# Performance work log

Measured on AMD Instinct MI355X. Metric: run time of the kernel, lower is better.

The kernel has to match this reference:

```python
import jax, jax.numpy as jnp
import numpy as np

DIM = 256
N_CHANNELS = 8
NEIGHBORS = 16


def setup_inputs() -> dict:
    key = jax.random.key(0)
    kx, kw = jax.random.split(key)
    B, N, D = 4, 1024, DIM
    x = jax.random.normal(kx, (B, N, D), dtype=jnp.float32)
    # nn.Linear(dim, dim*2*n_channels, bias=False); store as [in, out] so y = x @ W
    W_qk = jax.random.normal(kw, (D, 2 * N_CHANNELS * D), dtype=jnp.float32) * (D ** -0.5)
    return {"x": x, "W_qk": W_qk}


def _norm_edge(edge):
    # edge: [B, C, N, N]
    norm_row = edge / (edge.sum(axis=-1, keepdims=True) + 1e-6)
    norm_col = norm_row / (norm_row.sum(axis=-2, keepdims=True) + 1e-6)
    # norm_row @ norm_col^T
    return jnp.einsum('bcnk,bcmk->bcnm', norm_row, norm_col)


def reference(x, W_qk):
    B, N, D = x.shape
    C = N_CHANNELS
    scale = D ** -0.5
    qk = (x @ W_qk).reshape(B, N, 2, C, D)
    q = jnp.transpose(qk[:, :, 0], (0, 2, 1, 3))  # [B, C, N, D]
    k = jnp.transpose(qk[:, :, 1], (0, 2, 1, 3))  # [B, C, N, D]
    attn = jax.nn.softmax(jnp.einsum('bcnd,bcmd->bcnm', q, k) * scale, axis=-1)

    # clip(): top-k neighbor mask from channel-summed (detached) attention
    sum_edge = jax.lax.stop_gradient(attn).sum(axis=1)  # [B, N, N]
    kk = min(NEIGHBORS, N)
    _, top_idx = jax.lax.top_k(sum_edge, kk)  # [B, N, kk]
    b_idx = jnp.arange(B)[:, None, None]
    r_idx = jnp.arange(N)[None, :, None]
    mask = jnp.zeros((B, N, N), dtype=attn.dtype).at[b_idx, r_idx, top_idx].set(1.0)
    mask = jnp.maximum(mask, jnp.eye(N, dtype=attn.dtype))  # identity diag
    edge = mask[:, None] * attn  # [B, C, N, N]
    return _norm_edge(edge)
```

## Files before the change

kernel.cpp:

```cpp
#include <hip/hip_runtime.h>
#include <hip/hip_bf16.h>
#include <math.h>

#define BB 4
#define NN 1024
#define DD 256
#define CC 8
#define KNBR 16
#define MAXSEL 17
#define ZCAP (NN * MAXSEL)

typedef _Float16 f16x8_t __attribute__((ext_vector_type(8)));
typedef _Float16 f16x4_t __attribute__((ext_vector_type(4)));
typedef float    f32x4_t __attribute__((ext_vector_type(4)));

__device__ __forceinline__ void gl2lds16(const _Float16* g, _Float16* ldsbase) {
    __builtin_amdgcn_global_load_lds(
        (const __attribute__((address_space(1))) unsigned int*)g,
        (__attribute__((address_space(3))) unsigned int*)ldsbase, 16, 0, 0);
}

__device__ __forceinline__ void split2(float v, _Float16& h, _Float16& l) {
    h = (_Float16)v;
    l = (_Float16)(v - (float)h);
}

__global__ __launch_bounds__(256) void split_all(const float* __restrict__ x,
                                                 const float* __restrict__ W,
                                                 _Float16* __restrict__ xh,
                                                 _Float16* __restrict__ xl,
                                                 _Float16* __restrict__ Wth,
                                                 _Float16* __restrict__ Wtl,
                                                 int* __restrict__ countb) {
    const int tid = threadIdx.x;
    if (blockIdx.x < 1024) {
        int i = (blockIdx.x * 256 + tid) * 4;
        float4 v = *(const float4*)(x + i);
        f16x4_t hv, lv;
        _Float16 h, l;
        split2(v.x, h, l); hv[0] = h; lv[0] = l;
        split2(v.y, h, l); hv[1] = h; lv[1] = l;
        split2(v.z, h, l); hv[2] = h; lv[2] = l;
        split2(v.w, h, l); hv[3] = h; lv[3] = l;
        *(f16x4_t*)(xh + i) = hv;
        *(f16x4_t*)(xl + i) = lv;
    } else {
        const int b2 = blockIdx.x - 1024;
        if (b2 == 0) {
            int4 zz = make_int4(0, 0, 0, 0);
#pragma unroll
            for (int g = 0; g < 4; g++) ((int4*)countb)[tid + 256 * g] = zz;
        }
        __shared__ float t[64][65];
        const int n0 = (b2 & 63) * 64;
        const int k0 = (b2 >> 6) * 64;
#pragma unroll
        for (int i = 0; i < 16; i++) {
            int k = i * 4 + (tid >> 6);
            int n = tid & 63;
            t[k][n] = W[(size_t)(k0 + k) * 4096 + n0 + n];
        }
        __syncthreads();
#pragma unroll
        for (int i = 0; i < 16; i++) {
            int n = i * 4 + (tid >> 6);
            int k = tid & 63;
            _Float16 h, l;
            split2(t[k][n] * 16.f, h, l);
            size_t o = (size_t)(n0 + n) * 256 + k0 + k;
            Wth[o] = h; Wtl[o] = l;
        }
    }
}

#define STG(dst, src, rowbase, kk)                                             \
    do {                                                                       \
        gl2lds16((src) + (size_t)((rowbase) + r_st) * 256 + (kk) + c8,         \
                 &(dst)[(w * 64) * 8]);                                        \
        gl2lds16((src) + (size_t)((rowbase) + 64 + r_st) * 256 + (kk) + c8,    \
                 &(dst)[(256 + w * 64) * 8]);                                  \
    } while (0)

#define MFMA3(accv, AH, AL, BH, BL)                                            \
    do {                                                                       \
        accv = __builtin_amdgcn_mfma_f32_16x16x32_f16(AL, BH, accv, 0, 0, 0);  \
        accv = __builtin_amdgcn_mfma_f32_16x16x32_f16(AH, BL, accv, 0, 0, 0);  \
        accv = __builtin_amdgcn_mfma_f32_16x16x32_f16(AH, BH, accv, 0, 0, 0);  \
    } while (0)

#define COMPUTE(AH, AL, BH, BL)                                                \
    do {                                                                       \
        f16x8_t ah[4], al[4];                                                  \
        _Pragma("unroll")                                                      \
        for (int mi = 0; mi < 4; mi++) {                                       \
            int r = (wr * 64 + mi * 16 + lm) * 32 + qx8;                       \
            ah[mi] = *(const f16x8_t*)&(AH)[r];                                \
            al[mi] = *(const f16x8_t*)&(AL)[r];                                \
        }                                                                      \
        _Pragma("unroll")                                                      \
        for (int ni = 0; ni < 4; ni++) {                                       \
            int rb = (wc * 64 + ni * 16 + lm) * 32 + qx8;                      \
            f16x8_t bh = *(const f16x8_t*)&(BH)[rb];                           \
            f16x8_t bl = *(const f16x8_t*)&(BL)[rb];                           \
            _Pragma("unroll")                                                  \
            for (int mi = 0; mi < 4; mi++)                                     \
                MFMA3(acc[mi][ni], ah[mi], al[mi], bh, bl);                    \
        }                                                                      \
    } while (0)

__global__ __launch_bounds__(256) void gemm_xw_mfma(
        const _Float16* __restrict__ xh, const _Float16* __restrict__ xl,
        const _Float16* __restrict__ wth, const _Float16* __restrict__ wtl,
        _Float16* __restrict__ qh, _Float16* __restrict__ ql,
        _Float16* __restrict__ kh, _Float16* __restrict__ kl) {
    __shared__ __align__(16) char smem[65536];
    _Float16* Ah0 = (_Float16*)smem;
    _Float16* Al0 = (_Float16*)(smem + 8192);
    _Float16* Bh0 = (_Float16*)(smem + 16384);
    _Float16* Bl0 = (_Float16*)(smem + 24576);
    _Float16* Ah1 = (_Float16*)(smem + 32768);
    _Float16* Al1 = (_Float16*)(smem + 40960);
    _Float16* Bh1 = (_Float16*)(smem + 49152);
    _Float16* Bl1 = (_Float16*)(smem + 57344);
    const int tid = threadIdx.x, lane = tid & 63, w = tid >> 6;
    const int wr = w >> 1, wc = w & 1;
    const int lm = lane & 15, quad = lane >> 4;
    const int row0 = blockIdx.y * 128, col0 = blockIdx.x * 128;
    const int r_st = tid >> 2;
    const int c8 = (((tid & 3) ^ ((tid >> 3) & 3)) * 8);
    const int qx8 = ((quad ^ ((lm >> 1) & 3)) * 8);

    f32x4_t acc[4][4];
#pragma unroll
    for (int i = 0; i < 4; i++)
#pragma unroll
        for (int j = 0; j < 4; j++) acc[i][j] = (f32x4_t)(0.f);

    STG(Ah0, xh, row0, 0); STG(Al0, xl, row0, 0);
    STG(Bh0, wth, col0, 0); STG(Bl0, wtl, col0, 0);
    __syncthreads();
#pragma unroll
    for (int t = 0; t < 8; t += 2) {
        {
            int kn = (t + 1) * 32;
            if (t + 1 < 8) {
                STG(Ah1, xh, row0, kn); STG(Al1, xl, row0, kn);
                STG(Bh1, wth, col0, kn); STG(Bl1, wtl, col0, kn);
            }
            COMPUTE(Ah0, Al0, Bh0, Bl0);
            __syncthreads();
        }
        {
            int kn = (t + 2) * 32;
            if (t + 2 < 8) {
                STG(Ah0, xh, row0, kn); STG(Al0, xl, row0, kn);
                STG(Bh0, wth, col0, kn); STG(Bl0, wtl, col0, kn);
            }
            COMPUTE(Ah1, Al1, Bh1, Bl1);
            __syncthreads();
        }
    }

    float* tr = (float*)smem;
    const int s = col0 >> 11, c = (col0 >> 8) & 7, dbase = col0 & 255;
    _Float16* dh = s ? kh : qh;
    _Float16* dl = s ? kl : ql;
    const int rl = tid >> 2;
    const int cb = (tid & 3) * 8;
#pragma unroll
    for (int p = 0; p < 2; p++) {
        if (p) __syncthreads();
        if (wr == p) {
#pragma unroll
            for (int mi = 0; mi < 4; mi++) {
                int rloc = mi * 16 + quad * 4;
#pragma unroll
                for (int ni = 0; ni < 4; ni++) {
                    int cl = wc * 64 + ni * 16 + lm;
#pragma unroll
                    for (int r = 0; r < 4; r++)
                        tr[(rloc + r) * 132 + cl] = acc[mi][ni][r];
                }
            }
        }
        __syncthreads();
        int rr = row0 + p * 64 + rl;
        int bb = rr >> 10, n = rr & 1023;
        size_t base = (((size_t)(bb * CC + c)) * NN + n) * DD + dbase;
#pragma unroll
        for (int g = 0; g < 4; g++) {
            int ccol = g * 32 + cb;
            f16x8_t hv, lv;
#pragma unroll
            for (int e = 0; e < 8; e++) {
                float vv = tr[rl * 132 + ccol + e];
                _Float16 h, l;
                split2(vv, h, l);
                hv[e] = h; lv[e] = l;
            }
            *(f16x8_t*)(dh + base + ccol) = hv;
            *(f16x8_t*)(dl + base + ccol) = lv;
        }
    }
}

__global__ __launch_bounds__(256) void gemm_qkt_mfma(
        const _Float16* __restrict__ qh, const _Float16* __restrict__ ql,
        const _Float16* __restrict__ kh, const _Float16* __restrict__ kl,
        float* __restrict__ attn) {
    __shared__ __align__(16) char smem[65536];
    _Float16* Ah0 = (_Float16*)smem;
    _Float16* Al0 = (_Float16*)(smem + 8192);
    _Float16* Bh0 = (_Float16*)(smem + 16384);
    _Float16* Bl0 = (_Float16*)(smem + 24576);
    _Float16* Ah1 = (_Float16*)(smem + 32768);
    _Float16* Al1 = (_Float16*)(smem + 40960);
    _Float16* Bh1 = (_Float16*)(smem + 49152);
    _Float16* Bl1 = (_Float16*)(smem + 57344);
    const int tid = threadIdx.x, lane = tid & 63, w = tid >> 6;
    const int wr = w >> 1, wc = w & 1;
    const int lm = lane & 15, quad = lane >> 4;
    const int id = blockIdx.x;
    const int rb8 = id & 7, qq = id >> 3;
    const int j = qq & 63, zhi = qq >> 6;
    const int z = zhi * 8 + rb8;
    const int row0 = (j >> 3) * 128, col0 = (j & 7) * 128;
    const size_t zo = (size_t)z * NN * DD;
    float* Cm = attn + (size_t)z * NN * NN;
    const int r_st = tid >> 2;
    const int c8 = (((tid & 3) ^ ((tid >> 3) & 3)) * 8);
    const int qx8 = ((quad ^ ((lm >> 1) & 3)) * 8);
    const float scale = 0.0625f / 256.0f;

    f32x4_t acc[4][4];
#pragma unroll
    for (int i = 0; i < 4; i++)
#pragma unroll
        for (int j2 = 0; j2 < 4; j2++) acc[i][j2] = (f32x4_t)(0.f);

    const _Float16* qhz = qh + zo;
    const _Float16* qlz = ql + zo;
    const _Float16* khz = kh + zo;
    const _Float16* klz = kl + zo;

    STG(Ah0, qhz, row0, 0); STG(Al0, qlz, row0, 0);
    STG(Bh0, khz, col0, 0); STG(Bl0, klz, col0, 0);
    __syncthreads();
#pragma unroll
    for (int t = 0; t < 8; t += 2) {
        {
            int kn = (t + 1) * 32;
            if (t + 1 < 8) {
                STG(Ah1, qhz, row0, kn); STG(Al1, qlz, row0, kn);
                STG(Bh1, khz, col0, kn); STG(Bl1, klz, col0, kn);
            }
            COMPUTE(Ah0, Al0, Bh0, Bl0);
            __syncthreads();
        }
        {
            int kn = (t + 2) * 32;
            if (t + 2 < 8) {
                STG(Ah0, qhz, row0, kn); STG(Al0, qlz, row0, kn);
                STG(Bh0, khz, col0, kn); STG(Bl0, klz, col0, kn);
            }
            COMPUTE(Ah1, Al1, Bh1, Bl1);
            __syncthreads();
        }
    }

#pragma unroll
    for (int mi = 0; mi < 4; mi++)
#pragma unroll
        for (int ni = 0; ni < 4; ni++) {
            int row = row0 + wr * 64 + mi * 16 + quad * 4;
            int col = col0 + wc * 64 + ni * 16 + lm;
#pragma unroll
            for (int r = 0; r < 4; r++)
                Cm[(size_t)(row + r) * NN + col] = acc[mi][ni][r] * scale;
        }
}

__global__ __launch_bounds__(256) void softmax_topk(const float* __restrict__ attn,
                                                    float2* __restrict__ ml,
                                                    int* __restrict__ idx,
                                                    int* __restrict__ cnt,
                                                    int* __restrict__ countb,
                                                    float* __restrict__ colsum) {
    __shared__ float psum[4][1280];
    __shared__ int fsel[MAXSEL];
    __shared__ int fcnt;
    const int bn = blockIdx.x, b = bn >> 10, n = bn & 1023;
    const int tid = threadIdx.x, lane = tid & 63, w = tid >> 6;

    if (tid < CC) colsum[(size_t)(b * CC + tid) * NN + n] = 0.f;

    const int colb = lane * 16;
    const int pb   = lane * 20;
    float4 u[2][4];
#pragma unroll
    for (int p = 0; p < 2; p++) {
        const int c = w * 2 + p;
        const float* rowp = attn + (((size_t)(b * CC + c) * NN + n) * NN) + colb;
#pragma unroll
        for (int g = 0; g < 4; g++) u[p][g] = *(const float4*)(rowp + g * 4);
    }

    float acc[16];
#pragma unroll
    for (int e = 0; e < 16; e++) acc[e] = 0.f;

#pragma unroll
    for (int p = 0; p < 2; p++) {
        const int c = w * 2 + p;
        const float* f = (const float*)&u[p][0];
        float mx = f[0];
#pragma unroll
        for (int e = 1; e < 16; e++) mx = fmaxf(mx, f[e]);
#pragma unroll
        for (int off = 1; off < 64; off <<= 1) mx = fmaxf(mx, __shfl_xor(mx, off));
        float sm = 0.f;
        float pe[16];
#pragma unroll
        for (int e = 0; e < 16; e++) { pe[e] = expf(f[e] - mx); sm += pe[e]; }
#pragma unroll
        for (int off = 1; off < 64; off <<= 1) sm += __shfl_xor(sm, off);
        if (lane == 0) ml[(size_t)(b * CC + c) * NN + n] = make_float2(mx, sm);
        float inv = 1.0f / sm;
#pragma unroll
        for (int e = 0; e < 16; e++) acc[e] += pe[e] * inv;
    }
#pragma unroll
    for (int g = 0; g < 4; g++)
        *(float4*)&psum[w][pb + g * 4] =
            make_float4(acc[g * 4], acc[g * 4 + 1], acc[g * 4 + 2], acc[g * 4 + 3]);
    __syncthreads();

    const int p4 = tid * 4 + (tid >> 2) * 4;
    float4 a0 = *(const float4*)&psum[0][p4];
    float4 a1 = *(const float4*)&psum[1][p4];
    float4 a2 = *(const float4*)&psum[2][p4];
    float4 a3 = *(const float4*)&psum[3][p4];
    float4 vs;
    vs.x = a0.x + a1.x + a2.x + a3.x;
    vs.y = a0.y + a1.y + a2.y + a3.y;
    vs.z = a0.z + a1.z + a2.z + a3.z;
    vs.w = a0.w + a1.w + a2.w + a3.w;
    *(float4*)&psum[0][p4] = vs;
    __syncthreads();

    if (w == 0) {
        unsigned vb[16];
#pragma unroll
        for (int g = 0; g < 4; g++) {
            float4 t4 = *(const float4*)&psum[0][pb + g * 4];
            vb[g * 4 + 0] = __float_as_uint(t4.x);
            vb[g * 4 + 1] = __float_as_uint(t4.y);
            vb[g * 4 + 2] = __float_as_uint(t4.z);
            vb[g * 4 + 3] = __float_as_uint(t4.w);
        }
        unsigned lo = 0u, hi = 0x7F800000u;
        while (lo < hi) {
            unsigned mid = lo + ((hi - lo) >> 1);
            int c = 0;
#pragma unroll
            for (int e = 0; e < 16; e++)
                c += (int)__popcll(__ballot(vb[e] > mid));
            if (c <= 15) hi = mid; else lo = mid + 1;
        }
        const unsigned V = hi;
        int cgt = 0, ceq = 0;
#pragma unroll
        for (int e = 0; e < 16; e++) {
            cgt += (vb[e] > V) ? 1 : 0;
            ceq += (vb[e] == V) ? 1 : 0;
        }
        int pk = cgt | (ceq << 16);
        int incl = pk;
#pragma unroll
        for (int o = 1; o < 64; o <<= 1) {
            int v2 = __shfl_up(incl, o);
            if (lane >= o) incl += v2;
        }
        int tot = __shfl(incl, 63);
        int c1 = tot & 0xffff;
        int need = KNBR - c1;
        int excl = incl - pk;
        int pg = excl & 0xffff;
        int pe2 = excl >> 16;
        int lg = 0, le = 0;
#pragma unroll
        for (int e = 0; e < 16; e++) {
            if (vb[e] > V) {
                fsel[pg + lg] = colb + e; lg++;
            } else if (vb[e] == V) {
                if (pe2 + le < need) fsel[c1 + pe2 + le] = colb + e;
                le++;
            }
        }
        if (lane == 0) {
            bool has = false;
#pragma unroll
            for (int t2 = 0; t2 < KNBR; t2++)
                if (fsel[t2] == n) has = true;
            int c = KNBR;
            if (!has) { fsel[KNBR] = n; c = KNBR + 1; }
            fcnt = c;
            cnt[bn] = c;
        }
    }
    __syncthreads();
    if (tid < fcnt) {
        idx[bn * MAXSEL + tid] = fsel[tid];
        atomicAdd(&countb[b * NN + fsel[tid]], 1);
    }
}

__global__ __launch_bounds__(256) void scan_offb(const int* __restrict__ countb,
                                                 int* __restrict__ offb,
                                                 int* __restrict__ curs,
                                                 const int* __restrict__ cnt,
                                                 const int* __restrict__ idx,
                                                 int* __restrict__ eidx,
                                                 int* __restrict__ pmap) {
    __shared__ int wtot[4];
    const int b = blockIdx.x, tid = threadIdx.x, lane = tid & 63, w = tid >> 6;
    int c0 = countb[b * NN + tid * 4 + 0];
    int c1 = countb[b * NN + tid * 4 + 1];
    int c2 = countb[b * NN + tid * 4 + 2];
    int c3 = countb[b * NN + tid * 4 + 3];
    int tsum = c0 + c1 + c2 + c3;
    int incl = tsum;
#pragma unroll
    for (int off = 1; off < 64; off <<= 1) {
        int v = __shfl_up(incl, off);
        if (lane >= off) incl += v;
    }
    if (lane == 63) wtot[w] = incl;
    __syncthreads();
    int woff = 0;
    for (int i = 0; i < w; i++) woff += wtot[i];
    int base = woff + incl - tsum;
    int o0 = base, o1 = base + c0, o2 = base + c0 + c1, o3 = base + c0 + c1 + c2;
    offb[b * NN + tid * 4 + 0] = o0;
    offb[b * NN + tid * 4 + 1] = o1;
    offb[b * NN + tid * 4 + 2] = o2;
    offb[b * NN + tid * 4 + 3] = o3;
    curs[b * NN + tid * 4 + 0] = o0;
    curs[b * NN + tid * 4 + 1] = o1;
    curs[b * NN + tid * 4 + 2] = o2;
    curs[b * NN + tid * 4 + 3] = o3;
    __syncthreads();

    for (int r = 0; r < 4; r++) {
        int n = tid + r * 256;
        int bn = b * NN + n;
        int c_ = cnt[bn];
        int start = n & 15;
        for (int jj = 0; jj < MAXSEL; jj++) {
            if (jj < c_) {
                int j = jj + start;
                if (j >= c_) j -= c_;
                int k = idx[bn * MAXSEL + j];
                int p = atomicAdd(&curs[b * NN + k], 1);
                eidx[b * ZCAP + p] = n;
                pmap[bn * MAXSEL + j] = p;
            }
        }
    }
}

__global__ __launch_bounds__(256) void rownorm_fill(const float* __restrict__ attn,
                                                    const float2* __restrict__ ml,
                                                    const int* __restrict__ idx,
                                                    const int* __restrict__ cnt,
                                                    const int* __restrict__ pmap,
                                                    float* __restrict__ nr,
                                                    float* __restrict__ colsum,
                                                    float* __restrict__ eval8) {
    const int t = blockIdx.x * 256 + threadIdx.x;
    const int z = t >> 10, n = t & 1023;
    const int b = z >> 3, c = z & 7;
    const int bn = b * NN + n;
    const int c_ = cnt[bn];
    const float* arow = attn + (size_t)t * NN;
    const float2 MM = ml[t];
    const float invl = 1.0f / MM.y;
    float a[MAXSEL];
    int kk[MAXSEL];
    float s = 0.f;
#pragma unroll
    for (int j = 0; j < MAXSEL; j++) {
        if (j < c_) {
            kk[j] = idx[bn * MAXSEL + j];
            float p = expf(arow[kk[j]] - MM.x) * invl;
            a[j] = p; s += p;
        }
    }
    const float inv = 1.f / (s + 1e-6f);
#pragma unroll
    for (int j = 0; j < MAXSEL; j++) {
        if (j < c_) {
            float v = a[j] * inv;
            nr[(size_t)t * MAXSEL + j] = v;
            atomicAdd(&colsum[(size_t)z * NN + kk[j]], v);
            int p = pmap[bn * MAXSEL + j];
            eval8[((size_t)b * ZCAP + p) * 8 + c] = v;
        }
    }
}

__global__ __launch_bounds__(512) void out_sparse(const float* __restrict__ nr,
                                                  const int* __restrict__ idx,
                                                  const int* __restrict__ cnt,
                                                  const int* __restrict__ offb,
                                                  const int* __restrict__ countb,
                                                  const float* __restrict__ colsum,
                                                  const int* __restrict__ eidx,
                                                  const float* __restrict__ eval8,
                                                  float* __restrict__ out) {
    __shared__ float acc[CC][NN];
    __shared__ float scm[CC][MAXSEL];
    __shared__ int goffs[MAXSEL];
    __shared__ int glens[MAXSEL];
    const int bn = blockIdx.x;
    const int b = bn >> 10, n = bn & 1023;
    const int tid = threadIdx.x, lane = tid & 63, w = tid >> 6;
    const int c_ = cnt[bn];

    f32x4_t zz = (f32x4_t)(0.f);
#pragma unroll
    for (int q = 0; q < 4; q++) ((f32x4_t*)acc)[tid + q * 512] = zz;

    if (tid < 256) {
        int c = tid >> 5, j = tid & 31;
        if (j < MAXSEL) {
            float sc = 0.f;
            if (j < c_) {
                int z = b * CC + c;
                int k = idx[bn * MAXSEL + j];
                float wgt = nr[((size_t)z * NN + n) * MAXSEL + j];
                sc = wgt / (colsum[(size_t)z * NN + k] + 1e-6f);
            }
            scm[c][j] = sc;
        }
    } else if (tid < 256 + MAXSEL) {
        int j = tid - 256;
        int off = 0, len = 0;
        if (j < c_) {
            int k = idx[bn * MAXSEL + j];
            off = offb[b * NN + k];
            len = countb[b * NN + k];
        }
        goffs[j] = off; glens[j] = len;
    }
    __syncthreads();

    for (int j = w; j < c_; j += 8) {
        const int off = goffs[j], len = glens[j];
        const float s0 = scm[0][j], s1 = scm[1][j], s2 = scm[2][j], s3 = scm[3][j];
        const float s4 = scm[4][j], s5 = scm[5][j], s6 = scm[6][j], s7 = scm[7][j];
        for (int l = lane; l < len; l += 64) {
            int m = eidx[b * ZCAP + off + l];
            const float* vp = eval8 + ((size_t)b * ZCAP + off + l) * 8;
            f32x4_t va = *(const f32x4_t*)vp;
            f32x4_t vb2 = *(const f32x4_t*)(vp + 4);
            atomicAdd(&acc[0][m], s0 * va[0]);
            atomicAdd(&acc[1][m], s1 * va[1]);
            atomicAdd(&acc[2][m], s2 * va[2]);
            atomicAdd(&acc[3][m], s3 * va[3]);
            atomicAdd(&acc[4][m], s4 * vb2[0]);
            atomicAdd(&acc[5][m], s5 * vb2[1]);
            atomicAdd(&acc[6][m], s6 * vb2[2]);
            atomicAdd(&acc[7][m], s7 * vb2[3]);
        }
    }
    __syncthreads();

#pragma unroll
    for (int q = 0; q < 4; q++) {
        int i4 = tid + q * 512;
        int c = i4 >> 8, m4 = i4 & 255;
        *(f32x4_t*)(out + ((size_t)(b * CC + c) * NN + n) * NN + m4 * 4) =
            ((f32x4_t*)acc)[i4];
    }
}

extern "C" void kernel_launch(void* const* d_in, const int* in_sizes, int n_in,
                              void* d_out, int out_size, void* d_ws, size_t ws_size,
                              hipStream_t stream) {
    const float* x = (const float*)d_in[0];
    const float* W = (const float*)d_in[1];
    float* out = (float*)d_out;
    char* ws = (char*)d_ws;

    float* attn = (float*)d_out;

    _Float16* qh  = (_Float16*)(ws);
    _Float16* ql  = (_Float16*)(ws + 16777216ull);
    _Float16* kh  = (_Float16*)(ws + 33554432ull);
    _Float16* kl  = (_Float16*)(ws + 50331648ull);
    _Float16* xh  = (_Float16*)(ws + 67108864ull);
    _Float16* xl  = (_Float16*)(ws + 69206016ull);
    _Float16* wth = (_Float16*)(ws + 71303168ull);
    _Float16* wtl = (_Float16*)(ws + 73400320ull);
    int*    idx  = (int*)   (ws + 75497472ull);
    int*    cnt  = (int*)   (ws + 75776000ull);
    float*  nr   = (float*) (ws + 75792384ull);
    float*  colsum = (float*)(ws + 78020608ull);
    float2* ml   = (float2*)(ws + 78151680ull);
    int*    countb = (int*) (ws + 78413824ull);
    int*    offb = (int*)   (ws + 78430208ull);
    int*    curs = (int*)   (ws + 78446592ull);
    int*    eidx = (int*)   (ws + 78577664ull);
    float*  eval8 = (float*)(ws + 78856192ull);
    int*    pmap = (int*)   (ws + 81084416ull);

    split_all<<<1280, 256, 0, stream>>>(x, W, xh, xl, wth, wtl, countb);
    gemm_xw_mfma<<<dim3(32, 32), 256, 0, stream>>>(xh, xl, wth, wtl,
                                                   qh, ql, kh, kl);
    gemm_qkt_mfma<<<2048, 256, 0, stream>>>(qh, ql, kh, kl, attn);
    softmax_topk<<<4096, 256, 0, stream>>>(attn, ml, idx, cnt, countb, colsum);
    scan_offb<<<4, 256, 0, stream>>>(countb, offb, curs, cnt, idx, eidx, pmap);
    rownorm_fill<<<128, 256, 0, stream>>>(attn, ml, idx, cnt, pmap, nr, colsum,
                                          eval8);
    out_sparse<<<4096, 512, 0, stream>>>(nr, idx, cnt, offb, countb, colsum,
                                         eidx, eval8, out);
}
```

Baseline: 415.2 us.

## Split scatter fill into wider kernel and shrink edge arrays to 16-bit

```diff
diff --git a/kernel.cpp b/kernel.cpp
--- a/kernel.cpp
+++ b/kernel.cpp
@@ -417,11 +417,7 @@
 
 __global__ __launch_bounds__(256) void scan_offb(const int* __restrict__ countb,
                                                  int* __restrict__ offb,
-                                                 int* __restrict__ curs,
-                                                 const int* __restrict__ cnt,
-                                                 const int* __restrict__ idx,
-                                                 int* __restrict__ eidx,
-                                                 int* __restrict__ pmap) {
+                                                 int* __restrict__ curs) {
     __shared__ int wtot[4];
     const int b = blockIdx.x, tid = threadIdx.x, lane = tid & 63, w = tid >> 6;
     int c0 = countb[b * NN + tid * 4 + 0];
@@ -449,22 +445,26 @@
     curs[b * NN + tid * 4 + 1] = o1;
     curs[b * NN + tid * 4 + 2] = o2;
     curs[b * NN + tid * 4 + 3] = o3;
-    __syncthreads();
-
-    for (int r = 0; r < 4; r++) {
-        int n = tid + r * 256;
-        int bn = b * NN + n;
-        int c_ = cnt[bn];
-        int start = n & 15;
-        for (int jj = 0; jj < MAXSEL; jj++) {
-            if (jj < c_) {
-                int j = jj + start;
-                if (j >= c_) j -= c_;
-                int k = idx[bn * MAXSEL + j];
-                int p = atomicAdd(&curs[b * NN + k], 1);
-                eidx[b * ZCAP + p] = n;
-                pmap[bn * MAXSEL + j] = p;
-            }
+}
+
+__global__ __launch_bounds__(64) void fill_struct(const int* __restrict__ cnt,
+                                                  const int* __restrict__ idx,
+                                                  int* __restrict__ curs,
+                                                  unsigned short* __restrict__ eidx16,
+                                                  int* __restrict__ pmap) {
+    const int b = blockIdx.x >> 4;
+    const int n = ((blockIdx.x & 15) << 6) + threadIdx.x;
+    const int bn = b * NN + n;
+    const int c_ = cnt[bn];
+    const int start = n & 15;
+    for (int jj = 0; jj < MAXSEL; jj++) {
+        if (jj < c_) {
+            int j = jj + start;
+            if (j >= c_) j -= c_;
+            int k = idx[bn * MAXSEL + j];
+            int p = atomicAdd(&curs[b * NN + k], 1);
+            eidx16[b * ZCAP + p] = (unsigned short)n;
+            pmap[bn * MAXSEL + j] = p;
         }
     }
 }
@@ -476,7 +476,7 @@
                                                     const int* __restrict__ pmap,
                                                     float* __restrict__ nr,
                                                     float* __restrict__ colsum,
-                                                    float* __restrict__ eval8) {
+                                                    _Float16* __restrict__ eval8h) {
     const int t = blockIdx.x * 256 + threadIdx.x;
     const int z = t >> 10, n = t & 1023;
     const int b = z >> 3, c = z & 7;
@@ -504,7 +504,7 @@
             nr[(size_t)t * MAXSEL + j] = v;
             atomicAdd(&colsum[(size_t)z * NN + kk[j]], v);
             int p = pmap[bn * MAXSEL + j];
-            eval8[((size_t)b * ZCAP + p) * 8 + c] = v;
+            eval8h[((size_t)b * ZCAP + p) * 8 + c] = (_Float16)v;
         }
     }
 }
@@ -515,8 +515,8 @@
                                                   const int* __restrict__ offb,
                                                   const int* __restrict__ countb,
                                                   const float* __restrict__ colsum,
-                                                  const int* __restrict__ eidx,
-                                                  const float* __restrict__ eval8,
+                                                  const unsigned short* __restrict__ eidx16,
+                                                  const _Float16* __restrict__ eval8h,
                                                   float* __restrict__ out) {
     __shared__ float acc[CC][NN];
     __shared__ float scm[CC][MAXSEL];
@@ -560,18 +560,16 @@
         const float s0 = scm[0][j], s1 = scm[1][j], s2 = scm[2][j], s3 = scm[3][j];
         const float s4 = scm[4][j], s5 = scm[5][j], s6 = scm[6][j], s7 = scm[7][j];
         for (int l = lane; l < len; l += 64) {
-            int m = eidx[b * ZCAP + off + l];
-            const float* vp = eval8 + ((size_t)b * ZCAP + off + l) * 8;
-            f32x4_t va = *(const f32x4_t*)vp;
-            f32x4_t vb2 = *(const f32x4_t*)(vp + 4);
-            atomicAdd(&acc[0][m], s0 * va[0]);
-            atomicAdd(&acc[1][m], s1 * va[1]);
-            atomicAdd(&acc[2][m], s2 * va[2]);
-            atomicAdd(&acc[3][m], s3 * va[3]);
-            atomicAdd(&acc[4][m], s4 * vb2[0]);
-            atomicAdd(&acc[5][m], s5 * vb2[1]);
-            atomicAdd(&acc[6][m], s6 * vb2[2]);
-            atomicAdd(&acc[7][m], s7 * vb2[3]);
+            int m = eidx16[b * ZCAP + off + l];
+            f16x8_t vh = *(const f16x8_t*)(eval8h + ((size_t)b * ZCAP + off + l) * 8);
+            atomicAdd(&acc[0][m], s0 * (float)vh[0]);
+            atomicAdd(&acc[1][m], s1 * (float)vh[1]);
+            atomicAdd(&acc[2][m], s2 * (float)vh[2]);
+            atomicAdd(&acc[3][m], s3 * (float)vh[3]);
+            atomicAdd(&acc[4][m], s4 * (float)vh[4]);
+            atomicAdd(&acc[5][m], s5 * (float)vh[5]);
+            atomicAdd(&acc[6][m], s6 * (float)vh[6]);
+            atomicAdd(&acc[7][m], s7 * (float)vh[7]);
         }
     }
     __syncthreads();
@@ -611,18 +609,19 @@
     int*    countb = (int*) (ws + 78413824ull);
     int*    offb = (int*)   (ws + 78430208ull);
     int*    curs = (int*)   (ws + 78446592ull);
-    int*    eidx = (int*)   (ws + 78577664ull);
-    float*  eval8 = (float*)(ws + 78856192ull);
-    int*    pmap = (int*)   (ws + 81084416ull);
+    unsigned short* eidx16 = (unsigned short*)(ws + 78462976ull);
+    _Float16* eval8h = (_Float16*)(ws + 78602240ull);
+    int*    pmap = (int*)   (ws + 79716352ull);
 
     split_all<<<1280, 256, 0, stream>>>(x, W, xh, xl, wth, wtl, countb);
     gemm_xw_mfma<<<dim3(32, 32), 256, 0, stream>>>(xh, xl, wth, wtl,
                                                    qh, ql, kh, kl);
     gemm_qkt_mfma<<<2048, 256, 0, stream>>>(qh, ql, kh, kl, attn);
     softmax_topk<<<4096, 256, 0, stream>>>(attn, ml, idx, cnt, countb, colsum);
-    scan_offb<<<4, 256, 0, stream>>>(countb, offb, curs, cnt, idx, eidx, pmap);
+    scan_offb<<<4, 256, 0, stream>>>(countb, offb, curs);
+    fill_struct<<<64, 64, 0, stream>>>(cnt, idx, curs, eidx16, pmap);
     rownorm_fill<<<128, 256, 0, stream>>>(attn, ml, idx, cnt, pmap, nr, colsum,
-                                          eval8);
+                                          eval8h);
     out_sparse<<<4096, 512, 0, stream>>>(nr, idx, cnt, offb, countb, colsum,
-                                         eidx, eval8, out);
-}
+                                         eidx16, eval8h, out);
+}
```

Measured after the change: 378.6 us. -8.8%, faster.
